# Kernel optimization log

Hardware: AMD Instinct MI355X
Metric: run time of the kernel (lower is better)

The kernel has to match this reference:

```python
import jax, jax.numpy as jnp
import numpy as np

N = 50000          # residues
E = 1000000        # edges
H = 128            # hidden_channels
CUT = 11.5         # cutoff
NR = 6             # num_radial
NS = 3             # num_spherical
NPE = 16           # num_pos_emb

def swish(x):
    return x * jax.nn.sigmoid(x)

def rbf(d):
    # Bessel-style radial basis with smooth cosine cutoff, [E, NR]
    u = jnp.clip(d / CUT, 0.0, 1.0)
    n = jnp.arange(1, NR + 1, dtype=jnp.float32)
    fc = 0.5 * (jnp.cos(jnp.pi * u) + 1.0)
    return jnp.sqrt(2.0 / CUT) * jnp.sin(n * jnp.pi * u[:, None]) / (d[:, None] + 1e-6) * fc[:, None]

def angle_emb(d, ang):
    # d_angle_emb: radial x cos(l*angle) -> [E, NR*NS]
    r = rbf(d)
    l = jnp.arange(NS, dtype=jnp.float32)
    a = jnp.cos(ang[:, None] * l)
    return (r[:, :, None] * a[:, None, :]).reshape(d.shape[0], NR * NS)

def theta_phi_emb(d, theta, phi):
    # d_theta_phi_emb: radial x angular(theta) x angular(phi) -> [E, NR*NS*NS]
    r = rbf(d)
    l = jnp.arange(NS, dtype=jnp.float32)
    ct = jnp.cos(theta[:, None] * l)
    cp = jnp.cos(phi[:, None] * l)
    return jnp.einsum('en,el,em->enlm', r, ct, cp).reshape(d.shape[0], NR * NS * NS)


def setup_inputs():
    key = jax.random.key(0)
    ks = jax.random.split(key, 20)
    f32 = jnp.float32
    pos = jax.random.normal(ks[0], (N, 3), f32) * 8.0
    pos_n = pos + jax.random.normal(ks[1], (N, 3), f32) * 0.8
    pos_c = pos + jax.random.normal(ks[2], (N, 3), f32) * 0.8
    z = jax.random.randint(ks[3], (N,), 0, 26)
    bb_embs = jax.random.normal(ks[4], (N, 6), f32)
    side_chain_embs = jax.random.normal(ks[5], (N, 8), f32)
    esm_embs = jax.random.normal(ks[6], (N, 1280), f32)
    batch = jnp.zeros((N,), jnp.int32)
    edge_index = jax.random.randint(ks[7], (2, E), 0, N)
    def w(k, shape):
        return jax.random.normal(k, shape, f32) * (1.0 / np.sqrt(shape[0]))
    edge_in = NR * NS * NS + 3 * NR * NS + NPE  # 54 + 54 + 16 = 124
    params = dict(
        W_emb=w(ks[8], (26 + 6 + 8, H // 2)), b_emb=jnp.zeros((H // 2,), f32),
        W_esm=w(ks[9], (1280, H // 2)), b_esm=jnp.zeros((H // 2,), f32),
        W_edge=w(ks[10], (edge_in, H)),
        W_msg=w(ks[11], (H, H)),
        W_upd=w(ks[12], (H, H)),
        W_o0=w(ks[13], (H, H)), b_o0=jnp.zeros((H,), f32),
        W_o1=w(ks[14], (H, 32)), b_o1=jnp.zeros((32,), f32),
        W_of=w(ks[15], (32, 1)), b_of=jnp.zeros((1,), f32),
        W_n0=w(ks[16], (H, 32)), b_n0=jnp.zeros((32,), f32),
        W_nf=w(ks[17], (32, 2)), b_nf=jnp.zeros((2,), f32),
    )
    return dict(z=z, pos=pos, pos_n=pos_n, pos_c=pos_c, bb_embs=bb_embs,
                side_chain_embs=side_chain_embs, esm_embs=esm_embs,
                batch=batch, edge_index=edge_index, **params)


def reference(z, pos, pos_n, pos_c, bb_embs, side_chain_embs, esm_embs, batch,
              edge_index, W_emb, b_emb, W_esm, b_esm, W_edge, W_msg, W_upd,
              W_o0, b_o0, W_o1, b_o1, W_of, b_of, W_n0, b_n0, W_nf, b_nf):
    # --- node embedding fusion (level='allatom+esm') ---
    oh = jax.nn.one_hot(z, 26, dtype=jnp.float32)
    x_a = jnp.concatenate([oh, bb_embs, side_chain_embs], axis=1) @ W_emb + b_emb
    x_s = esm_embs @ W_esm + b_esm
    x = jnp.concatenate([x_a, x_s], axis=-1)  # [N, H]

    j, i = edge_index[0], edge_index[1]

    # --- sinusoidal positional embedding of sequence offsets ---
    dpe = (j - i).astype(jnp.float32)
    freq = jnp.exp(jnp.arange(0, NPE, 2, dtype=jnp.float32) * (-np.log(10000.0) / NPE))
    ang = dpe[:, None] * freq
    pe = jnp.concatenate([jnp.cos(ang), jnp.sin(ang)], axis=-1)  # [E, NPE]

    # --- distance / theta / phi (triplet gathers via sequence neighbors) ---
    v_ji = pos[j] - pos[i]
    dist = jnp.linalg.norm(pos[i] - pos[j], axis=1)
    refi0 = (i - 1) % N
    refi1 = (i + 1) % N
    v_r0 = pos[refi0] - pos[i]
    v_r1 = pos[refi1] - pos[i]
    a = jnp.sum(v_ji * v_r0, axis=-1)
    b = jnp.linalg.norm(jnp.cross(v_ji, v_r0), axis=-1)
    theta = jnp.arctan2(b, a)
    p1 = jnp.cross(v_r0, v_r1)
    p2 = jnp.cross(v_r0, v_ji)
    a = jnp.sum(p1 * p2, axis=-1)
    b = jnp.sum(jnp.cross(p1, p2) * v_r0, axis=-1) / (jnp.linalg.norm(v_r0, axis=-1) + 1e-7)
    phi = jnp.arctan2(b, a)
    feature0 = theta_phi_emb(dist, theta, phi)  # [E, 54]

    # --- backbone-frame Euler angles (allatom branch) ---
    o1x = pos_n[i] - pos[i]
    o1z = jnp.cross(o1x, jnp.cross(o1x, pos_c[i] - pos[i]))
    o1zl = jnp.linalg.norm(o1z, axis=1) + 1e-7
    o2x = pos_n[j] - pos[j]
    o2z = jnp.cross(o2x, jnp.cross(o2x, pos_c[j] - pos[j]))
    o2zl = jnp.linalg.norm(o2z, axis=1) + 1e-7
    nvec = jnp.cross(o1z, o2z)
    angle1 = jnp.arctan2(jnp.sum(jnp.cross(o1x, nvec) * o1z, -1) / o1zl, jnp.sum(o1x * nvec, -1))
    angle2 = jnp.arctan2(jnp.linalg.norm(nvec, axis=-1), jnp.sum(o1z * o2z, -1))
    angle3 = jnp.arctan2(jnp.sum(jnp.cross(nvec, o2x) * o2z, -1) / o2zl, jnp.sum(nvec * o2x, -1))
    feature1 = jnp.concatenate([angle_emb(dist, angle1), angle_emb(dist, angle2),
                                angle_emb(dist, angle3)], axis=1)  # [E, 54]

    # --- message passing (gather-compute-scatter stand-in for model_E) ---
    ef = swish(jnp.concatenate([feature0, feature1, pe], axis=-1) @ W_edge)  # [E, H]
    m = swish(x[j] @ W_msg) * ef
    agg = jax.ops.segment_sum(m, i, num_segments=N)
    xe = x + swish(agg @ W_upd)

    # --- output heads (dropout inactive at inference) ---
    xn = jax.nn.relu(x @ W_n0 + b_n0)
    node_out = xn @ W_nf + b_nf                   # [N, 2]
    h = jax.nn.relu(xe @ W_o0 + b_o0)
    h = jax.nn.relu(h @ W_o1 + b_o1)
    out = jax.nn.sigmoid(h @ W_of + b_of)         # [N, 1]
    return out, node_out
```

## Files before the change

### kernel.cpp

```cpp
#include <hip/hip_runtime.h>
#include <math.h>
#include <stdint.h>

#define NRES 50000
#define NEDGE 1000000
#define PI_F 3.14159265358979323846f
#define NSEG 196

typedef __attribute__((ext_vector_type(8))) short short8;
typedef __attribute__((ext_vector_type(4))) float floatx4;
typedef __attribute__((ext_vector_type(2))) short bf16x2;
typedef __attribute__((address_space(1))) bf16x2* gbf16x2p;

struct f3 { float x, y, z; };
__device__ __forceinline__ f3 ld3(const float* __restrict__ p, int i) {
  return {p[3*i+0], p[3*i+1], p[3*i+2]};
}
__device__ __forceinline__ f3 f3sub(f3 a, f3 b){ return {a.x-b.x, a.y-b.y, a.z-b.z}; }
__device__ __forceinline__ f3 f3cross(f3 a, f3 b){
  return {a.y*b.z - a.z*b.y, a.z*b.x - a.x*b.z, a.x*b.y - a.y*b.x};
}
__device__ __forceinline__ float f3dot(f3 a, f3 b){ return a.x*b.x + a.y*b.y + a.z*b.z; }
__device__ __forceinline__ float swish_fast(float v){
  return v * __builtin_amdgcn_rcpf(1.0f + __expf(-v));
}
__device__ __forceinline__ short f2bf(float f){
  unsigned u = __float_as_uint(f);
  unsigned r = (u + 0x7fffu + ((u >> 16) & 1u)) >> 16;
  return (short)r;
}
__device__ __forceinline__ float bf2f(short s){
  return __uint_as_float(((unsigned)(unsigned short)s) << 16);
}
__device__ __forceinline__ float cos_atan2(float y, float x){
  return x * __builtin_amdgcn_rsqf(fmaxf(x*x + y*y, 1e-30f));
}
__device__ __forceinline__ void atom_pk_bf16(short* addr, bf16x2 v){
  __builtin_amdgcn_global_atomic_fadd_v2bf16((gbf16x2p)(uintptr_t)addr, v);
}
__device__ __forceinline__ unsigned pkbf(float lo, float hi){
  unsigned r;
  asm("v_cvt_pk_bf16_f32 %0, %1, %2" : "=v"(r) : "v"(lo), "v"(hi));
  return r;
}

__device__ __forceinline__ void edge_features(
    int e, int j, int i,
    const float* __restrict__ pos, const float* __restrict__ posn,
    const float* __restrict__ posc, short (*sF)[136])
{
  f3 pj = ld3(pos, j), pi = ld3(pos, i);
  f3 vji = f3sub(pj, pi);
  float nji2 = f3dot(vji, vji);
  float dist = sqrtf(nji2);
  int r0i = (i == 0) ? (NRES - 1) : (i - 1);
  int r1i = (i == NRES - 1) ? 0 : (i + 1);
  f3 vr0 = f3sub(ld3(pos, r0i), pi);
  f3 vr1 = f3sub(ld3(pos, r1i), pi);
  float nr02 = f3dot(vr0, vr0);

  float ct = f3dot(vji, vr0) * __builtin_amdgcn_rsqf(fmaxf(nji2 * nr02, 1e-30f));
  f3 p1 = f3cross(vr0, vr1);
  f3 p2 = f3cross(vr0, vji);
  float pa = f3dot(p1, p2);
  float pb = f3dot(f3cross(p1, p2), vr0) / (sqrtf(nr02) + 1e-7f);
  float cp = cos_atan2(pb, pa);

  f3 pni = ld3(posn, i), pci = ld3(posc, i);
  f3 o1x = f3sub(pni, pi);
  f3 o1z = f3cross(o1x, f3cross(o1x, f3sub(pci, pi)));
  float no1z2 = f3dot(o1z, o1z);
  float o1zl = sqrtf(no1z2) + 1e-7f;
  f3 pnj = ld3(posn, j), pcj = ld3(posc, j);
  f3 o2x = f3sub(pnj, pj);
  f3 o2z = f3cross(o2x, f3cross(o2x, f3sub(pcj, pj)));
  float no2z2 = f3dot(o2z, o2z);
  float o2zl = sqrtf(no2z2) + 1e-7f;
  f3 nv = f3cross(o1z, o2z);
  float y1 = f3dot(f3cross(o1x, nv), o1z) / o1zl;
  float ca1 = cos_atan2(y1, f3dot(o1x, nv));
  float ca2 = f3dot(o1z, o2z) * __builtin_amdgcn_rsqf(fmaxf(no1z2 * no2z2, 1e-30f));
  float y3 = f3dot(f3cross(nv, o2x), o2z) / o2zl;
  float ca3 = cos_atan2(y3, f3dot(nv, o2x));

  float u = fminf(dist * (1.0f/11.5f), 1.0f);
  float spu, cpu;
  __sincosf(PI_F * u, &spu, &cpu);
  float fc = 0.5f * (cpu + 1.0f);
  float pref = 0.41702882811414954f * __builtin_amdgcn_rcpf(dist + 1e-6f) * fc;
  float rb[6];
  {
    float twoc = 2.0f * cpu;
    float s_nm1 = 0.0f, s_n = spu;
    #pragma unroll
    for (int nn = 0; nn < 6; ++nn) {
      rb[nn] = pref * s_n;
      float s_np1 = twoc * s_n - s_nm1;
      s_nm1 = s_n; s_n = s_np1;
    }
  }

  float pend = 0.0f;
  float ctv[3] = {1.0f, ct, 2.0f*ct*ct - 1.0f};
  float cpv[3] = {1.0f, cp, 2.0f*cp*cp - 1.0f};
  #pragma unroll
  for (int nn = 0; nn < 6; ++nn)
    #pragma unroll
    for (int l = 0; l < 3; ++l)
      #pragma unroll
      for (int m = 0; m < 3; ++m) {
        const int f = nn*9 + l*3 + m;
        float v = rb[nn] * ctv[l] * cpv[m];
        if (f & 1) *(unsigned*)&sF[e][f-1] = pkbf(pend, v);
        else       pend = v;
      }

  float cas[3] = {ca1, ca2, ca3};
  #pragma unroll
  for (int t = 0; t < 3; ++t) {
    float c = cas[t];
    float cav[3] = {1.0f, c, 2.0f*c*c - 1.0f};
    #pragma unroll
    for (int nn = 0; nn < 6; ++nn)
      #pragma unroll
      for (int l = 0; l < 3; ++l) {
        const int f = 54 + t*18 + nn*3 + l;
        float v = rb[nn] * cav[l];
        if (f & 1) *(unsigned*)&sF[e][f-1] = pkbf(pend, v);
        else       pend = v;
      }
  }

  const float FRQ[8] = {1.0f, 0.31622776601683794f, 0.1f, 0.03162277660168379f,
                        0.01f, 0.003162277660168379f, 0.001f, 0.0003162277660168379f};
  float dpe = (float)(j - i);
  float cb[8], sb[8];
  #pragma unroll
  for (int q = 0; q < 8; ++q) __sincosf(dpe * FRQ[q], &sb[q], &cb[q]);
  #pragma unroll
  for (int q = 0; q < 8; q += 2) {
    *(unsigned*)&sF[e][108 + q] = pkbf(cb[q], cb[q+1]);
    *(unsigned*)&sF[e][116 + q] = pkbf(sb[q], sb[q+1]);
  }
  *(unsigned*)&sF[e][124] = 0u;
  *(unsigned*)&sF[e][126] = 0u;
}

__global__ __launch_bounds__(256) void k_wprep(
    const float* __restrict__ We, const float* __restrict__ Wm,
    const float* __restrict__ Ws, const float* __restrict__ Wu,
    const float* __restrict__ Wo0, const float* __restrict__ Wn0,
    const float* __restrict__ Wo1,
    short* __restrict__ Wef, short* __restrict__ Wmf, short* __restrict__ Wsf,
    short* __restrict__ Wuf, short* __restrict__ Wo0f,
    short* __restrict__ Wn0f, short* __restrict__ Wo1f)
{
  int gid = blockIdx.x * 256 + threadIdx.x;
  const float* src; short* dst; int NT, K, N, t;
  if      (gid < 16384)  { t = gid;          src = We;  dst = Wef;  NT = 8; K = 124;  N = 128; }
  else if (gid < 32768)  { t = gid - 16384;  src = Wm;  dst = Wmf;  NT = 8; K = 128;  N = 128; }
  else if (gid < 114688) { t = gid - 32768;  src = Ws;  dst = Wsf;  NT = 4; K = 1280; N = 64;  }
  else if (gid < 131072) { t = gid - 114688; src = Wu;  dst = Wuf;  NT = 8; K = 128;  N = 128; }
  else if (gid < 147456) { t = gid - 131072; src = Wo0; dst = Wo0f; NT = 8; K = 128;  N = 128; }
  else if (gid < 151552) { t = gid - 147456; src = Wn0; dst = Wn0f; NT = 2; K = 128;  N = 32;  }
  else if (gid < 155648) { t = gid - 151552; src = Wo1; dst = Wo1f; NT = 2; K = 128;  N = 32;  }
  else return;
  int j = t & 7, lane = (t >> 3) & 63;
  int rest = t >> 9;
  int nt = rest % NT, kt = rest / NT;
  int k = kt*32 + (lane >> 4)*8 + j, n = nt*16 + (lane & 15);
  dst[t] = f2bf((k < K) ? src[k*N + n] : 0.0f);
}

__global__ __launch_bounds__(256) void k_hist(
    const int* __restrict__ ei, int* __restrict__ bins)
{
  int e = blockIdx.x * 256 + threadIdx.x;
  if (e < NEDGE) atomicAdd(&bins[ei[NEDGE + e]], 1);
}

__global__ __launch_bounds__(256) void k_scan1(
    int* __restrict__ bins, int* __restrict__ bsum)
{
  __shared__ int s[256];
  const int t = threadIdx.x, b = blockIdx.x;
  const int idx = b * 256 + t;
  int v = (idx < NRES) ? bins[idx] : 0;
  s[t] = v;
  __syncthreads();
  #pragma unroll
  for (int d = 1; d < 256; d <<= 1) {
    int add = (t >= d) ? s[t - d] : 0;
    __syncthreads();
    if (t >= d) s[t] += add;
    __syncthreads();
  }
  if (idx < NRES) bins[idx] = s[t] - v;
  if (t == 255) bsum[b] = s[255];
}

__global__ __launch_bounds__(256) void k_scan2(int* __restrict__ bsum)
{
  __shared__ int s[256];
  const int t = threadIdx.x;
  int v = (t < NSEG) ? bsum[t] : 0;
  s[t] = v;
  __syncthreads();
  #pragma unroll
  for (int d = 1; d < 256; d <<= 1) {
    int add = (t >= d) ? s[t - d] : 0;
    __syncthreads();
    if (t >= d) s[t] += add;
    __syncthreads();
  }
  if (t < NSEG) bsum[t] = s[t] - v;
}

__global__ __launch_bounds__(256) void k_scan3(
    int* __restrict__ bins, const int* __restrict__ bsum)
{
  int idx = blockIdx.x * 256 + threadIdx.x;
  if (idx < NRES) bins[idx] += bsum[blockIdx.x];
}

__global__ __launch_bounds__(256) void k_scatter(
    const int* __restrict__ ei, int* __restrict__ bins, int2* __restrict__ sij)
{
  int e = blockIdx.x * 256 + threadIdx.x;
  if (e < NEDGE) {
    int j = ei[e], i = ei[NEDGE + e];
    int slot = atomicAdd(&bins[i], 1);
    if (slot >= 0 && slot < NEDGE) sij[slot] = make_int2(j, i);
  }
}

__global__ __launch_bounds__(256) void k_xa(
    const int* __restrict__ z, const float* __restrict__ bb,
    const float* __restrict__ side, const float* __restrict__ W_emb,
    const float* __restrict__ b_emb, short* __restrict__ xb)
{
  int tid = threadIdx.x;
  int h = tid & 63;
  int n = blockIdx.x * 4 + (tid >> 6);
  if (n >= NRES) return;
  int zz = z[n];
  float acc = W_emb[zz * 64 + h] + b_emb[h];
  #pragma unroll
  for (int k = 0; k < 6; ++k) acc += bb[n*6 + k] * W_emb[(26 + k)*64 + h];
  #pragma unroll
  for (int k = 0; k < 8; ++k) acc += side[n*8 + k] * W_emb[(32 + k)*64 + h];
  xb[(size_t)n * 128 + h] = f2bf(acc);
}

__global__ __launch_bounds__(256) void k_esm(
    const float* __restrict__ esm, const short* __restrict__ Wsf,
    const float* __restrict__ b, short* __restrict__ xb)
{
  const int tid = threadIdx.x;
  const int lane = tid & 63, w = tid >> 6;
  const int quad = lane >> 4, colb = lane & 15;
  const int tile0 = blockIdx.x * 64 + w * 16;

  int arow = tile0 + colb;
  if (arow >= NRES) arow = NRES - 1;
  const float* ap = esm + (size_t)arow * 1280 + quad * 8;

  floatx4 acc[4];
  #pragma unroll
  for (int nt = 0; nt < 4; ++nt) acc[nt] = (floatx4){0.f, 0.f, 0.f, 0.f};

  for (int kt = 0; kt < 40; ++kt) {
    float4 v0 = *(const float4*)(ap + kt*32);
    float4 v1 = *(const float4*)(ap + kt*32 + 4);
    short8 a;
    a[0] = f2bf(v0.x); a[1] = f2bf(v0.y); a[2] = f2bf(v0.z); a[3] = f2bf(v0.w);
    a[4] = f2bf(v1.x); a[5] = f2bf(v1.y); a[6] = f2bf(v1.z); a[7] = f2bf(v1.w);
    #pragma unroll
    for (int nt = 0; nt < 4; ++nt) {
      short8 bf = *(const short8*)&Wsf[(size_t)((kt*4 + nt)*64 + lane)*8];
      acc[nt] = __builtin_amdgcn_mfma_f32_16x16x32_bf16(a, bf, acc[nt], 0, 0, 0);
    }
  }
  #pragma unroll
  for (int nt = 0; nt < 4; ++nt) {
    int ch = nt*16 + colb;
    float bias = b[ch];
    #pragma unroll
    for (int r = 0; r < 4; ++r) {
      int n = tile0 + quad*4 + r;
      if (n < NRES) xb[(size_t)n * 128 + 64 + ch] = f2bf(acc[nt][r] + bias);
    }
  }
}

__global__ __launch_bounds__(512) void k_node(
    const float* __restrict__ esm, const short* __restrict__ Wsf,
    const float* __restrict__ b_esm,
    const int* __restrict__ z, const float* __restrict__ bb,
    const float* __restrict__ side, const float* __restrict__ W_emb,
    const float* __restrict__ b_emb,
    const short* __restrict__ Wmf,
    short* __restrict__ xb, short* __restrict__ xmb)
{
  __shared__ __align__(16) short sX[64][136];
  __shared__ float sP[4][16][68];

  const int tid = threadIdx.x;
  const int lane = tid & 63, w = tid >> 6;
  const int quad = lane >> 4, colb = lane & 15;
  const int t = w & 3, kh = w >> 2;
  const int n0 = blockIdx.x * 64;
  const int tile0 = n0 + t * 16;

  int arow = tile0 + colb;
  if (arow >= NRES) arow = NRES - 1;
  const float* ap = esm + (size_t)arow * 1280 + kh * 640 + quad * 8;

  floatx4 acc[4];
  #pragma unroll
  for (int nt = 0; nt < 4; ++nt) acc[nt] = (floatx4){0.f, 0.f, 0.f, 0.f};

  float4 v0 = *(const float4*)(ap);
  float4 v1 = *(const float4*)(ap + 4);
  for (int kt = 0; kt < 20; ++kt) {
    float4 nv0 = v0, nv1 = v1;
    if (kt < 19) {
      nv0 = *(const float4*)(ap + (kt+1)*32);
      nv1 = *(const float4*)(ap + (kt+1)*32 + 4);
    }
    short8 a;
    a[0] = f2bf(v0.x); a[1] = f2bf(v0.y); a[2] = f2bf(v0.z); a[3] = f2bf(v0.w);
    a[4] = f2bf(v1.x); a[5] = f2bf(v1.y); a[6] = f2bf(v1.z); a[7] = f2bf(v1.w);
    const int kc = kh*20 + kt;
    #pragma unroll
    for (int nt = 0; nt < 4; ++nt) {
      short8 bf = *(const short8*)&Wsf[(size_t)((kc*4 + nt)*64 + lane)*8];
      acc[nt] = __builtin_amdgcn_mfma_f32_16x16x32_bf16(a, bf, acc[nt], 0, 0, 0);
    }
    v0 = nv0; v1 = nv1;
  }

  if (kh == 1) {
    #pragma unroll
    for (int nt = 0; nt < 4; ++nt)
      #pragma unroll
      for (int r = 0; r < 4; ++r)
        sP[t][quad*4 + r][nt*16 + colb] = acc[nt][r];
  }
  __syncthreads();

  if (kh == 0) {
    #pragma unroll
    for (int nt = 0; nt < 4; ++nt) {
      int ch = nt*16 + colb;
      float bias = b_esm[ch];
      #pragma unroll
      for (int r = 0; r < 4; ++r)
        sX[t*16 + quad*4 + r][64 + ch] =
            f2bf(acc[nt][r] + sP[t][quad*4 + r][ch] + bias);
    }
  }
  {
    int r2 = tid >> 3;
    int n2 = n0 + r2; if (n2 >= NRES) n2 = NRES - 1;
    int c0 = (tid & 7) * 8;
    int zz = z[n2];
    float bbv[6], sdv[8];
    #pragma unroll
    for (int k = 0; k < 6; ++k) bbv[k] = bb[n2*6 + k];
    #pragma unroll
    for (int k = 0; k < 8; ++k) sdv[k] = side[n2*8 + k];
    #pragma unroll
    for (int c = 0; c < 8; c += 2) {
      float u0, u1;
      #pragma unroll
      for (int h = 0; h < 2; ++h) {
        int col = c0 + c + h;
        float a2 = W_emb[zz*64 + col] + b_emb[col];
        #pragma unroll
        for (int k = 0; k < 6; ++k) a2 += bbv[k] * W_emb[(26 + k)*64 + col];
        #pragma unroll
        for (int k = 0; k < 8; ++k) a2 += sdv[k] * W_emb[(32 + k)*64 + col];
        if (h) u1 = a2; else u0 = a2;
      }
      *(unsigned*)&sX[r2][c0 + c] = pkbf(u0, u1);
    }
  }
  __syncthreads();

  #pragma unroll
  for (int it = 0; it < 2; ++it) {
    int idx = it * 512 + tid;
    int row = idx >> 4, c8 = idx & 15;
    int n = n0 + row;
    if (n < NRES) *(short8*)&xb[(size_t)n * 128 + c8*8] = *(const short8*)&sX[row][c8*8];
  }

  floatx4 accM[4];
  #pragma unroll
  for (int mt = 0; mt < 4; ++mt) accM[mt] = (floatx4){0.f,0.f,0.f,0.f};
  #pragma unroll
  for (int kt = 0; kt < 4; ++kt) {
    short8 b0 = *(const short8*)&Wmf[(size_t)((kt*8 + w)*64 + lane)*8];
    #pragma unroll
    for (int mt = 0; mt < 4; ++mt) {
      short8 a = *(const short8*)&sX[mt*16 + colb][kt*32 + quad*8];
      accM[mt] = __builtin_amdgcn_mfma_f32_16x16x32_bf16(a, b0, accM[mt], 0, 0, 0);
    }
  }
  __syncthreads();

  #pragma unroll
  for (int mt = 0; mt < 4; ++mt)
    #pragma unroll
    for (int r = 0; r < 4; ++r)
      sX[mt*16 + quad*4 + r][w*16 + colb] = f2bf(swish_fast(accM[mt][r]));
  __syncthreads();
  #pragma unroll
  for (int it = 0; it < 2; ++it) {
    int idx = it * 512 + tid;
    int row = idx >> 4, c8 = idx & 15;
    int n = n0 + row;
    if (n < NRES) *(short8*)&xmb[(size_t)n * 128 + c8*8] = *(const short8*)&sX[row][c8*8];
  }
}

__global__ __launch_bounds__(256, 4) void k_edge_s(
    const int2* __restrict__ sij,
    const float* __restrict__ pos,
    const float* __restrict__ posn, const float* __restrict__ posc,
    const short* __restrict__ xmb, const short* __restrict__ Wef,
    short* __restrict__ aggb)
{
  __shared__ int sJ[64];
  __shared__ int sI[64];
  __shared__ __align__(16) short sF[64][136];
  __shared__ __align__(16) short sXJ[64][136];

  const int tid = threadIdx.x;
  const int orig = blockIdx.x;
  const int xcd = orig & 7, sub = orig >> 3;
  const int wg = (xcd == 0 ? 0 : 1954 + (xcd - 1) * 1953) + sub;
  const int e0 = wg * 64;

  if (tid < 64) {
    int2 ji = sij[e0 + tid];
    int jj = ji.x, ii = ji.y;
    sJ[tid] = (jj < 0) ? 0 : ((jj >= NRES) ? NRES - 1 : jj);
    sI[tid] = (ii < 0) ? 0 : ((ii >= NRES) ? NRES - 1 : ii);
  }
  __syncthreads();

  if (tid < 64) {
    edge_features(tid, sJ[tid], sI[tid], pos, posn, posc, sF);
  } else {
    const int t2 = tid - 64;
    for (int it = 0; it < 6; ++it) {
      int idx = it * 192 + t2;
      if (idx < 1024) {
        int row = idx >> 4;
        int c8 = idx & 15;
        *(short8*)&sXJ[row][c8*8] = *(const short8*)&xmb[(size_t)sJ[row] * 128 + c8*8];
      }
    }
  }
  __syncthreads();

  const int lane = tid & 63, w = tid >> 6;
  const int quad = lane >> 4, colb = lane & 15;
  const int nb = w * 2;

  short8 bE[4][2];
  #pragma unroll
  for (int kt = 0; kt < 4; ++kt)
    #pragma unroll
    for (int nt = 0; nt < 2; ++nt)
      bE[kt][nt] = *(const short8*)&Wef[(size_t)((kt*8 + nb + nt)*64 + lane)*8];

  floatx4 accE[4][2];
  #pragma unroll
  for (int mt = 0; mt < 4; ++mt) {
    accE[mt][0] = (floatx4){0.f, 0.f, 0.f, 0.f};
    accE[mt][1] = (floatx4){0.f, 0.f, 0.f, 0.f};
  }

  #pragma unroll
  for (int kt = 0; kt < 4; ++kt) {
    #pragma unroll
    for (int mt = 0; mt < 4; ++mt) {
      short8 af = *(const short8*)&sF[mt*16 + colb][kt*32 + quad*8];
      #pragma unroll
      for (int nt = 0; nt < 2; ++nt)
        accE[mt][nt] = __builtin_amdgcn_mfma_f32_16x16x32_bf16(af, bE[kt][nt], accE[mt][nt], 0, 0, 0);
    }
  }
  __syncthreads();

  short (*sM)[136] = sF;
  #pragma unroll
  for (int mt = 0; mt < 4; ++mt)
    #pragma unroll
    for (int nt = 0; nt < 2; ++nt) {
      int ch = w*32 + nt*16 + colb;
      #pragma unroll
      for (int r = 0; r < 4; ++r) {
        int e = mt*16 + quad*4 + r;
        float mv = bf2f(sXJ[e][ch]) * swish_fast(accE[mt][nt][r]);
        sM[e][ch] = f2bf(mv);
      }
    }
  __syncthreads();

  {
    const int p = tid & 63;
    const int g = tid >> 6;
    float ax = 0.f, ay = 0.f;
    int cur = sI[g * 16];
    #pragma unroll
    for (int rr = 0; rr < 16; ++rr) {
      int row = g * 16 + rr;
      int ii = sI[row];
      if (ii != cur) {
        bf16x2 v; v[0] = f2bf(ax); v[1] = f2bf(ay);
        atom_pk_bf16(&aggb[(size_t)cur * 128 + p*2], v);
        ax = 0.f; ay = 0.f; cur = ii;
      }
      bf16x2 mv = *(const bf16x2*)&sM[row][p*2];
      ax += bf2f(mv[0]); ay += bf2f(mv[1]);
    }
    bf16x2 v; v[0] = f2bf(ax); v[1] = f2bf(ay);
    atom_pk_bf16(&aggb[(size_t)cur * 128 + p*2], v);
  }
}

__global__ __launch_bounds__(256, 4) void k_edge_b(
    const int* __restrict__ ei, const float* __restrict__ pos,
    const float* __restrict__ posn, const float* __restrict__ posc,
    const short* __restrict__ xb, const short* __restrict__ Wef,
    const short* __restrict__ Wmf, short* __restrict__ aggb)
{
  __shared__ int sJ[64];
  __shared__ int sI[64];
  __shared__ __align__(16) short sF[64][136];
  __shared__ __align__(16) short sXJ[64][136];

  const int tid = threadIdx.x;
  const int e0 = blockIdx.x * 64;

  if (tid < 64) { sJ[tid] = ei[e0 + tid]; sI[tid] = ei[NEDGE + e0 + tid]; }
  __syncthreads();

  if (tid < 64) {
    edge_features(tid, sJ[tid], sI[tid], pos, posn, posc, sF);
  } else {
    const int t2 = tid - 64;
    for (int it = 0; it < 6; ++it) {
      int idx = it * 192 + t2;
      if (idx < 1024) {
        int row = idx >> 4;
        int c8 = idx & 15;
        *(short8*)&sXJ[row][c8*8] = *(const short8*)&xb[(size_t)sJ[row] * 128 + c8*8];
      }
    }
  }
  __syncthreads();

  const int lane = tid & 63, w = tid >> 6;
  const int quad = lane >> 4, colb = lane & 15;
  const int nb = w * 2;

  short8 bE[4][2], bM[4][2];
  #pragma unroll
  for (int kt = 0; kt < 4; ++kt)
    #pragma unroll
    for (int nt = 0; nt < 2; ++nt) {
      bE[kt][nt] = *(const short8*)&Wef[(size_t)((kt*8 + nb + nt)*64 + lane)*8];
      bM[kt][nt] = *(const short8*)&Wmf[(size_t)((kt*8 + nb + nt)*64 + lane)*8];
    }

  floatx4 accE[4][2], accM[4][2];
  #pragma unroll
  for (int mt = 0; mt < 4; ++mt)
    #pragma unroll
    for (int nt = 0; nt < 2; ++nt) {
      accE[mt][nt] = (floatx4){0.f, 0.f, 0.f, 0.f};
      accM[mt][nt] = (floatx4){0.f, 0.f, 0.f, 0.f};
    }

  #pragma unroll
  for (int kt = 0; kt < 4; ++kt) {
    #pragma unroll
    for (int mt = 0; mt < 4; ++mt) {
      short8 af = *(const short8*)&sF [mt*16 + colb][kt*32 + quad*8];
      short8 ax = *(const short8*)&sXJ[mt*16 + colb][kt*32 + quad*8];
      #pragma unroll
      for (int nt = 0; nt < 2; ++nt) {
        accE[mt][nt] = __builtin_amdgcn_mfma_f32_16x16x32_bf16(af, bE[kt][nt], accE[mt][nt], 0, 0, 0);
        accM[mt][nt] = __builtin_amdgcn_mfma_f32_16x16x32_bf16(ax, bM[kt][nt], accM[mt][nt], 0, 0, 0);
      }
    }
  }
  __syncthreads();

  short (*sM)[136] = sXJ;
  #pragma unroll
  for (int mt = 0; mt < 4; ++mt)
    #pragma unroll
    for (int nt = 0; nt < 2; ++nt) {
      int ch = w*32 + nt*16 + colb;
      #pragma unroll
      for (int r = 0; r < 4; ++r) {
        int e = mt*16 + quad*4 + r;
        sM[e][ch] = f2bf(swish_fast(accM[mt][nt][r]) * swish_fast(accE[mt][nt][r]));
      }
    }
  __syncthreads();

  #pragma unroll
  for (int it = 0; it < 16; ++it) {
    int flat = it * 256 + tid;
    int row = flat >> 6, p = flat & 63;
    bf16x2 v = *(const bf16x2*)&sM[row][p*2];
    atom_pk_bf16(&aggb[(size_t)sI[row] * 128 + p*2], v);
  }
}

__global__ __launch_bounds__(256) void k_upd(
    const short* __restrict__ xb, const short* __restrict__ aggb,
    const short* __restrict__ Wuf, const short* __restrict__ Wo0f,
    const short* __restrict__ Wn0f, const short* __restrict__ Wo1f,
    const float* __restrict__ bn0, const float* __restrict__ Wnf,
    const float* __restrict__ bnf, const float* __restrict__ bo0,
    const float* __restrict__ bo1, const float* __restrict__ Wof,
    const float* __restrict__ bof, float* __restrict__ out0,
    float* __restrict__ out1)
{
  __shared__ __align__(16) short sA[64][136];
  __shared__ __align__(16) short sX[64][136];
  __shared__ float sS[64][33];

  const int tid = threadIdx.x;
  const int lane = tid & 63, w = tid >> 6;
  const int quad = lane >> 4, colb = lane & 15;
  const int n0 = blockIdx.x * 64;

  #pragma unroll
  for (int it = 0; it < 4; ++it) {
    int idx = it * 256 + tid;
    int row = idx >> 4, c8 = idx & 15;
    int n = n0 + row;
    short8 va = (short8)(short)0, vx = (short8)(short)0;
    if (n < NRES) {
      va = *(const short8*)&aggb[(size_t)n * 128 + c8*8];
      vx = *(const short8*)&xb  [(size_t)n * 128 + c8*8];
    }
    *(short8*)&sA[row][c8*8] = va;
    *(short8*)&sX[row][c8*8] = vx;
  }
  __syncthreads();

  {
    floatx4 accN[2];
    accN[0] = (floatx4){0.f,0.f,0.f,0.f}; accN[1] = (floatx4){0.f,0.f,0.f,0.f};
    #pragma unroll
    for (int kt = 0; kt < 4; ++kt) {
      short8 a = *(const short8*)&sX[w*16 + colb][kt*32 + quad*8];
      #pragma unroll
      for (int nt = 0; nt < 2; ++nt) {
        short8 bf = *(const short8*)&Wn0f[(size_t)((kt*2 + nt)*64 + lane)*8];
        accN[nt] = __builtin_amdgcn_mfma_f32_16x16x32_bf16(a, bf, accN[nt], 0, 0, 0);
      }
    }
    #pragma unroll
    for (int nt = 0; nt < 2; ++nt) {
      int col = nt*16 + colb;
      float bias = bn0[col];
      #pragma unroll
      for (int r = 0; r < 4; ++r)
        sS[w*16 + quad*4 + r][col] = fmaxf(accN[nt][r] + bias, 0.0f);
    }
  }
  __syncthreads();
  if (tid < 128) {
    int row = tid >> 1, oc = tid & 1;
    int n = n0 + row;
    if (n < NRES) {
      float a2 = bnf[oc];
      #pragma unroll
      for (int k = 0; k < 32; ++k) a2 += sS[row][k] * Wnf[k*2 + oc];
      out1[(size_t)n * 2 + oc] = a2;
    }
  }

  floatx4 acc1[4][2];
  #pragma unroll
  for (int mt = 0; mt < 4; ++mt) {
    acc1[mt][0] = (floatx4){0.f,0.f,0.f,0.f};
    acc1[mt][1] = (floatx4){0.f,0.f,0.f,0.f};
  }
  #pragma unroll
  for (int kt = 0; kt < 4; ++kt) {
    short8 b0 = *(const short8*)&Wuf[(size_t)((kt*8 + w*2 + 0)*64 + lane)*8];
    short8 b1 = *(const short8*)&Wuf[(size_t)((kt*8 + w*2 + 1)*64 + lane)*8];
    #pragma unroll
    for (int mt = 0; mt < 4; ++mt) {
      short8 a = *(const short8*)&sA[mt*16 + colb][kt*32 + quad*8];
      acc1[mt][0] = __builtin_amdgcn_mfma_f32_16x16x32_bf16(a, b0, acc1[mt][0], 0, 0, 0);
      acc1[mt][1] = __builtin_amdgcn_mfma_f32_16x16x32_bf16(a, b1, acc1[mt][1], 0, 0, 0);
    }
  }
  __syncthreads();
  #pragma unroll
  for (int mt = 0; mt < 4; ++mt)
    #pragma unroll
    for (int nt = 0; nt < 2; ++nt)
      #pragma unroll
      for (int r = 0; r < 4; ++r) {
        int row = mt*16 + quad*4 + r, col = w*32 + nt*16 + colb;
        float xv = bf2f(sX[row][col]);
        sA[row][col] = f2bf(xv + swish_fast(acc1[mt][nt][r]));
      }
  __syncthreads();

  floatx4 acc2[4][2];
  #pragma unroll
  for (int mt = 0; mt < 4; ++mt) {
    acc2[mt][0] = (floatx4){0.f,0.f,0.f,0.f};
    acc2[mt][1] = (floatx4){0.f,0.f,0.f,0.f};
  }
  #pragma unroll
  for (int kt = 0; kt < 4; ++kt) {
    short8 b0 = *(const short8*)&Wo0f[(size_t)((kt*8 + w*2 + 0)*64 + lane)*8];
    short8 b1 = *(const short8*)&Wo0f[(size_t)((kt*8 + w*2 + 1)*64 + lane)*8];
    #pragma unroll
    for (int mt = 0; mt < 4; ++mt) {
      short8 a = *(const short8*)&sA[mt*16 + colb][kt*32 + quad*8];
      acc2[mt][0] = __builtin_amdgcn_mfma_f32_16x16x32_bf16(a, b0, acc2[mt][0], 0, 0, 0);
      acc2[mt][1] = __builtin_amdgcn_mfma_f32_16x16x32_bf16(a, b1, acc2[mt][1], 0, 0, 0);
    }
  }
  __syncthreads();
  #pragma unroll
  for (int mt = 0; mt < 4; ++mt)
    #pragma unroll
    for (int nt = 0; nt < 2; ++nt) {
      int col = w*32 + nt*16 + colb;
      float bias = bo0[col];
      #pragma unroll
      for (int r = 0; r < 4; ++r) {
        int row = mt*16 + quad*4 + r;
        sX[row][col] = f2bf(fmaxf(acc2[mt][nt][r] + bias, 0.0f));
      }
    }
  __syncthreads();

  {
    floatx4 accH[2];
    accH[0] = (floatx4){0.f,0.f,0.f,0.f}; accH[1] = (floatx4){0.f,0.f,0.f,0.f};
    #pragma unroll
    for (int kt = 0; kt < 4; ++kt) {
      short8 a = *(const short8*)&sX[w*16 + colb][kt*32 + quad*8];
      #pragma unroll
      for (int nt = 0; nt < 2; ++nt) {
        short8 bf = *(const short8*)&Wo1f[(size_t)((kt*2 + nt)*64 + lane)*8];
        accH[nt] = __builtin_amdgcn_mfma_f32_16x16x32_bf16(a, bf, accH[nt], 0, 0, 0);
      }
    }
    __syncthreads();
    #pragma unroll
    for (int nt = 0; nt < 2; ++nt) {
      int col = nt*16 + colb;
      float bias = bo1[col];
      #pragma unroll
      for (int r = 0; r < 4; ++r)
        sS[w*16 + quad*4 + r][col] = fmaxf(accH[nt][r] + bias, 0.0f);
    }
  }
  __syncthreads();

  if (tid < 64) {
    int n = n0 + tid;
    if (n < NRES) {
      float a2 = bof[0];
      #pragma unroll
      for (int k = 0; k < 32; ++k) a2 += sS[tid][k] * Wof[k];
      out0[n] = 1.0f / (1.0f + expf(-a2));
    }
  }
}

extern "C" void kernel_launch(void* const* d_in, const int* in_sizes, int n_in,
                              void* d_out, int out_size, void* d_ws, size_t ws_size,
                              hipStream_t stream) {
  (void)in_sizes; (void)n_in; (void)out_size;
  const int*   z     = (const int*)  d_in[0];
  const float* pos   = (const float*)d_in[1];
  const float* posn  = (const float*)d_in[2];
  const float* posc  = (const float*)d_in[3];
  const float* bb    = (const float*)d_in[4];
  const float* side  = (const float*)d_in[5];
  const float* esm   = (const float*)d_in[6];
  const int*   ei    = (const int*)  d_in[8];
  const float* W_emb = (const float*)d_in[9];
  const float* b_emb = (const float*)d_in[10];
  const float* W_esm = (const float*)d_in[11];
  const float* b_esm = (const float*)d_in[12];
  const float* W_edge= (const float*)d_in[13];
  const float* W_msg = (const float*)d_in[14];
  const float* W_upd = (const float*)d_in[15];
  const float* W_o0  = (const float*)d_in[16];
  const float* b_o0  = (const float*)d_in[17];
  const float* W_o1  = (const float*)d_in[18];
  const float* b_o1  = (const float*)d_in[19];
  const float* W_of  = (const float*)d_in[20];
  const float* b_of  = (const float*)d_in[21];
  const float* W_n0  = (const float*)d_in[22];
  const float* b_n0  = (const float*)d_in[23];
  const float* W_nf  = (const float*)d_in[24];
  const float* b_nf  = (const float*)d_in[25];

  float* out0 = (float*)d_out;
  float* out1 = out0 + NRES;
  char* ws = (char*)d_ws;

  const bool full = (ws_size >= (size_t)46912096);

  if (full) {
    short* xb   = (short*)ws;
    short* aggb = (short*)(ws + 12800000);
    short* xmb  = (short*)(ws + 25600000);
    short* Wef  = (short*)(ws + 38400000);
    short* Wmf  = (short*)(ws + 38432768);
    short* Wsf  = (short*)(ws + 38465536);
    short* Wuf  = (short*)(ws + 38629376);
    short* Wo0f = (short*)(ws + 38662144);
    short* Wn0f = (short*)(ws + 38694912);
    short* Wo1f = (short*)(ws + 38703104);
    int*   bins = (int*)  (ws + 38711296);
    int*   bsum = (int*)  (ws + 38911296);
    int2*  sij  = (int2*) (ws + 38912096);

    hipMemsetAsync(aggb, 0, (size_t)NRES * 128 * sizeof(short), stream);
    hipMemsetAsync(bins, 0, (size_t)NRES * sizeof(int), stream);

    k_wprep  <<<608, 256, 0, stream>>>(W_edge, W_msg, W_esm, W_upd, W_o0, W_n0, W_o1,
                                       Wef, Wmf, Wsf, Wuf, Wo0f, Wn0f, Wo1f);
    k_hist   <<<3907, 256, 0, stream>>>(ei, bins);
    k_scan1  <<<NSEG, 256, 0, stream>>>(bins, bsum);
    k_scan2  <<<1,    256, 0, stream>>>(bsum);
    k_scan3  <<<NSEG, 256, 0, stream>>>(bins, bsum);
    k_scatter<<<3907, 256, 0, stream>>>(ei, bins, sij);
    k_node   <<<782,  512, 0, stream>>>(esm, Wsf, b_esm, z, bb, side, W_emb, b_emb,
                                        Wmf, xb, xmb);
    k_edge_s <<<15625, 256, 0, stream>>>(sij, pos, posn, posc, xmb, Wef, aggb);
    k_upd    <<<782,   256, 0, stream>>>(xb, aggb, Wuf, Wo0f, Wn0f, Wo1f,
                                         b_n0, W_nf, b_nf, b_o0, b_o1, W_of, b_of,
                                         out0, out1);
  } else {
    short* xb   = (short*)ws;
    short* aggb = (short*)(ws + 12800000);
    short* Wef  = (short*)(ws + 25600000);
    short* Wmf  = (short*)(ws + 25632768);
    short* Wsf  = (short*)(ws + 25665536);
    short* Wuf  = (short*)(ws + 25829376);
    short* Wo0f = (short*)(ws + 25862144);
    short* Wn0f = (short*)(ws + 25894912);
    short* Wo1f = (short*)(ws + 25903104);

    hipMemsetAsync(aggb, 0, (size_t)NRES * 128 * sizeof(short), stream);

    k_wprep <<<608, 256, 0, stream>>>(W_edge, W_msg, W_esm, W_upd, W_o0, W_n0, W_o1,
                                      Wef, Wmf, Wsf, Wuf, Wo0f, Wn0f, Wo1f);
    k_xa    <<<12500, 256, 0, stream>>>(z, bb, side, W_emb, b_emb, xb);
    k_esm   <<<782,   256, 0, stream>>>(esm, Wsf, b_esm, xb);
    k_edge_b<<<15625, 256, 0, stream>>>(ei, pos, posn, posc, xb, Wef, Wmf, aggb);
    k_upd   <<<782,   256, 0, stream>>>(xb, aggb, Wuf, Wo0f, Wn0f, Wo1f,
                                        b_n0, W_nf, b_nf, b_o0, b_o1, W_of, b_of,
                                        out0, out1);
  }
}
```

Before: 706.7 us.

## Split edge feature work across all warps, restage ESM GEMM, fold scan3 into scatter

In the sorted-edge kernel, each edge's features are now computed by four threads. Every thread recomputes the geometry and then writes one quarter of the feature row, replacing the old scheme where a single warp did all the feature math while the others gathered xmb. The node kernel's ESM projection now stages bf16-converted ESM rows in double-buffered shared memory with a 4x2 warp tiling over rows and columns, replacing the split-K approach and its partial-sum reduction. The k_scan3 launch is removed by adding the block offset during the scatter atomic. The cost is that the geometry is recomputed four times per edge, and the node kernel gains extra barriers.

```diff
diff --git a/kernel.cpp b/kernel.cpp
--- a/kernel.cpp
+++ b/kernel.cpp
@@ -44,11 +44,17 @@
   return r;
 }
 
-__device__ __forceinline__ void edge_features(
-    int e, int j, int i,
+struct EdgeGeo {
+  float rb[6];
+  float ct, cp, ca1, ca2, ca3;
+  float dpe;
+};
+__device__ __forceinline__ EdgeGeo edge_geo(
+    int j, int i,
     const float* __restrict__ pos, const float* __restrict__ posn,
-    const float* __restrict__ posc, short (*sF)[136])
-{
+    const float* __restrict__ posc)
+{
+  EdgeGeo g;
   f3 pj = ld3(pos, j), pi = ld3(pos, i);
   f3 vji = f3sub(pj, pi);
   float nji2 = f3dot(vji, vji);
@@ -59,12 +65,12 @@
   f3 vr1 = f3sub(ld3(pos, r1i), pi);
   float nr02 = f3dot(vr0, vr0);
 
-  float ct = f3dot(vji, vr0) * __builtin_amdgcn_rsqf(fmaxf(nji2 * nr02, 1e-30f));
+  g.ct = f3dot(vji, vr0) * __builtin_amdgcn_rsqf(fmaxf(nji2 * nr02, 1e-30f));
   f3 p1 = f3cross(vr0, vr1);
   f3 p2 = f3cross(vr0, vji);
   float pa = f3dot(p1, p2);
   float pb = f3dot(f3cross(p1, p2), vr0) / (sqrtf(nr02) + 1e-7f);
-  float cp = cos_atan2(pb, pa);
+  g.cp = cos_atan2(pb, pa);
 
   f3 pni = ld3(posn, i), pci = ld3(posc, i);
   f3 o1x = f3sub(pni, pi);
@@ -78,65 +84,68 @@
   float o2zl = sqrtf(no2z2) + 1e-7f;
   f3 nv = f3cross(o1z, o2z);
   float y1 = f3dot(f3cross(o1x, nv), o1z) / o1zl;
-  float ca1 = cos_atan2(y1, f3dot(o1x, nv));
-  float ca2 = f3dot(o1z, o2z) * __builtin_amdgcn_rsqf(fmaxf(no1z2 * no2z2, 1e-30f));
+  g.ca1 = cos_atan2(y1, f3dot(o1x, nv));
+  g.ca2 = f3dot(o1z, o2z) * __builtin_amdgcn_rsqf(fmaxf(no1z2 * no2z2, 1e-30f));
   float y3 = f3dot(f3cross(nv, o2x), o2z) / o2zl;
-  float ca3 = cos_atan2(y3, f3dot(nv, o2x));
+  g.ca3 = cos_atan2(y3, f3dot(nv, o2x));
 
   float u = fminf(dist * (1.0f/11.5f), 1.0f);
   float spu, cpu;
   __sincosf(PI_F * u, &spu, &cpu);
   float fc = 0.5f * (cpu + 1.0f);
   float pref = 0.41702882811414954f * __builtin_amdgcn_rcpf(dist + 1e-6f) * fc;
-  float rb[6];
   {
     float twoc = 2.0f * cpu;
     float s_nm1 = 0.0f, s_n = spu;
     #pragma unroll
     for (int nn = 0; nn < 6; ++nn) {
-      rb[nn] = pref * s_n;
+      g.rb[nn] = pref * s_n;
       float s_np1 = twoc * s_n - s_nm1;
       s_nm1 = s_n; s_n = s_np1;
     }
   }
-
-  float pend = 0.0f;
-  float ctv[3] = {1.0f, ct, 2.0f*ct*ct - 1.0f};
-  float cpv[3] = {1.0f, cp, 2.0f*cp*cp - 1.0f};
-  #pragma unroll
-  for (int nn = 0; nn < 6; ++nn)
-    #pragma unroll
-    for (int l = 0; l < 3; ++l)
-      #pragma unroll
-      for (int m = 0; m < 3; ++m) {
-        const int f = nn*9 + l*3 + m;
-        float v = rb[nn] * ctv[l] * cpv[m];
-        if (f & 1) *(unsigned*)&sF[e][f-1] = pkbf(pend, v);
-        else       pend = v;
-      }
-
-  float cas[3] = {ca1, ca2, ca3};
-  #pragma unroll
-  for (int t = 0; t < 3; ++t) {
-    float c = cas[t];
-    float cav[3] = {1.0f, c, 2.0f*c*c - 1.0f};
-    #pragma unroll
-    for (int nn = 0; nn < 6; ++nn)
-      #pragma unroll
-      for (int l = 0; l < 3; ++l) {
-        const int f = 54 + t*18 + nn*3 + l;
-        float v = rb[nn] * cav[l];
-        if (f & 1) *(unsigned*)&sF[e][f-1] = pkbf(pend, v);
-        else       pend = v;
-      }
-  }
-
+  g.dpe = (float)(j - i);
+  return g;
+}
+
+__device__ __forceinline__ float feat_val(const EdgeGeo& g, int f,
+                                          const float* ctv, const float* cpv,
+                                          const float* cav1, const float* cav2,
+                                          const float* cav3)
+{
+  if (f < 54) {
+    int nn = f / 9, l = (f % 9) / 3, m = f % 3;
+    return g.rb[nn] * ctv[l] * cpv[m];
+  } else {
+    int ff = f - 54;
+    int t = ff / 18, nn = (ff % 18) / 3, l = ff % 3;
+    const float* cav = (t == 0) ? cav1 : (t == 1) ? cav2 : cav3;
+    return g.rb[nn] * cav[l];
+  }
+}
+
+__device__ __forceinline__ void edge_features_full(
+    int e, int j, int i,
+    const float* __restrict__ pos, const float* __restrict__ posn,
+    const float* __restrict__ posc, short (*sF)[136])
+{
+  EdgeGeo g = edge_geo(j, i, pos, posn, posc);
+  float ctv[3]  = {1.0f, g.ct,  2.0f*g.ct*g.ct  - 1.0f};
+  float cpv[3]  = {1.0f, g.cp,  2.0f*g.cp*g.cp  - 1.0f};
+  float cav1[3] = {1.0f, g.ca1, 2.0f*g.ca1*g.ca1 - 1.0f};
+  float cav2[3] = {1.0f, g.ca2, 2.0f*g.ca2*g.ca2 - 1.0f};
+  float cav3[3] = {1.0f, g.ca3, 2.0f*g.ca3*g.ca3 - 1.0f};
+  #pragma unroll
+  for (int f = 0; f < 108; f += 2) {
+    float v0 = feat_val(g, f,     ctv, cpv, cav1, cav2, cav3);
+    float v1 = feat_val(g, f + 1, ctv, cpv, cav1, cav2, cav3);
+    *(unsigned*)&sF[e][f] = pkbf(v0, v1);
+  }
   const float FRQ[8] = {1.0f, 0.31622776601683794f, 0.1f, 0.03162277660168379f,
                         0.01f, 0.003162277660168379f, 0.001f, 0.0003162277660168379f};
-  float dpe = (float)(j - i);
   float cb[8], sb[8];
   #pragma unroll
-  for (int q = 0; q < 8; ++q) __sincosf(dpe * FRQ[q], &sb[q], &cb[q]);
+  for (int q = 0; q < 8; ++q) __sincosf(g.dpe * FRQ[q], &sb[q], &cb[q]);
   #pragma unroll
   for (int q = 0; q < 8; q += 2) {
     *(unsigned*)&sF[e][108 + q] = pkbf(cb[q], cb[q+1]);
@@ -144,6 +153,53 @@
   }
   *(unsigned*)&sF[e][124] = 0u;
   *(unsigned*)&sF[e][126] = 0u;
+}
+
+__device__ __forceinline__ void edge_features_q(
+    int e, int j, int i, int q,
+    const float* __restrict__ pos, const float* __restrict__ posn,
+    const float* __restrict__ posc, short (*sF)[136])
+{
+  EdgeGeo g = edge_geo(j, i, pos, posn, posc);
+  float ctv[3]  = {1.0f, g.ct,  2.0f*g.ct*g.ct  - 1.0f};
+  float cpv[3]  = {1.0f, g.cp,  2.0f*g.cp*g.cp  - 1.0f};
+  float cav1[3] = {1.0f, g.ca1, 2.0f*g.ca1*g.ca1 - 1.0f};
+  float cav2[3] = {1.0f, g.ca2, 2.0f*g.ca2*g.ca2 - 1.0f};
+  float cav3[3] = {1.0f, g.ca3, 2.0f*g.ca3*g.ca3 - 1.0f};
+
+  if (q == 0) {
+    #pragma unroll
+    for (int f = 0; f < 28; f += 2)
+      *(unsigned*)&sF[e][f] = pkbf(feat_val(g, f, ctv, cpv, cav1, cav2, cav3),
+                                   feat_val(g, f+1, ctv, cpv, cav1, cav2, cav3));
+  } else if (q == 1) {
+    #pragma unroll
+    for (int f = 28; f < 54; f += 2)
+      *(unsigned*)&sF[e][f] = pkbf(feat_val(g, f, ctv, cpv, cav1, cav2, cav3),
+                                   feat_val(g, f+1, ctv, cpv, cav1, cav2, cav3));
+    const float FRQ[8] = {1.0f, 0.31622776601683794f, 0.1f, 0.03162277660168379f,
+                          0.01f, 0.003162277660168379f, 0.001f, 0.0003162277660168379f};
+    float cb[8], sb[8];
+    #pragma unroll
+    for (int p = 0; p < 8; ++p) __sincosf(g.dpe * FRQ[p], &sb[p], &cb[p]);
+    #pragma unroll
+    for (int p = 0; p < 8; p += 2) {
+      *(unsigned*)&sF[e][108 + p] = pkbf(cb[p], cb[p+1]);
+      *(unsigned*)&sF[e][116 + p] = pkbf(sb[p], sb[p+1]);
+    }
+    *(unsigned*)&sF[e][124] = 0u;
+    *(unsigned*)&sF[e][126] = 0u;
+  } else if (q == 2) {
+    #pragma unroll
+    for (int f = 54; f < 80; f += 2)
+      *(unsigned*)&sF[e][f] = pkbf(feat_val(g, f, ctv, cpv, cav1, cav2, cav3),
+                                   feat_val(g, f+1, ctv, cpv, cav1, cav2, cav3));
+  } else {
+    #pragma unroll
+    for (int f = 80; f < 108; f += 2)
+      *(unsigned*)&sF[e][f] = pkbf(feat_val(g, f, ctv, cpv, cav1, cav2, cav3),
+                                   feat_val(g, f+1, ctv, cpv, cav1, cav2, cav3));
+  }
 }
 
 __global__ __launch_bounds__(256) void k_wprep(
@@ -216,20 +272,14 @@
   if (t < NSEG) bsum[t] = s[t] - v;
 }
 
-__global__ __launch_bounds__(256) void k_scan3(
-    int* __restrict__ bins, const int* __restrict__ bsum)
-{
-  int idx = blockIdx.x * 256 + threadIdx.x;
-  if (idx < NRES) bins[idx] += bsum[blockIdx.x];
-}
-
 __global__ __launch_bounds__(256) void k_scatter(
-    const int* __restrict__ ei, int* __restrict__ bins, int2* __restrict__ sij)
+    const int* __restrict__ ei, int* __restrict__ bins,
+    const int* __restrict__ bsum, int2* __restrict__ sij)
 {
   int e = blockIdx.x * 256 + threadIdx.x;
   if (e < NEDGE) {
     int j = ei[e], i = ei[NEDGE + e];
-    int slot = atomicAdd(&bins[i], 1);
+    int slot = atomicAdd(&bins[i], 1) + bsum[i >> 8];
     if (slot >= 0 && slot < NEDGE) sij[slot] = make_int2(j, i);
   }
 }
@@ -302,62 +352,70 @@
     const short* __restrict__ Wmf,
     short* __restrict__ xb, short* __restrict__ xmb)
 {
+  __shared__ __align__(16) short sE[2][64][72];
   __shared__ __align__(16) short sX[64][136];
-  __shared__ float sP[4][16][68];
 
   const int tid = threadIdx.x;
   const int lane = tid & 63, w = tid >> 6;
   const int quad = lane >> 4, colb = lane & 15;
-  const int t = w & 3, kh = w >> 2;
   const int n0 = blockIdx.x * 64;
-  const int tile0 = n0 + t * 16;
-
-  int arow = tile0 + colb;
-  if (arow >= NRES) arow = NRES - 1;
-  const float* ap = esm + (size_t)arow * 1280 + kh * 640 + quad * 8;
-
-  floatx4 acc[4];
-  #pragma unroll
-  for (int nt = 0; nt < 4; ++nt) acc[nt] = (floatx4){0.f, 0.f, 0.f, 0.f};
-
-  float4 v0 = *(const float4*)(ap);
-  float4 v1 = *(const float4*)(ap + 4);
-  for (int kt = 0; kt < 20; ++kt) {
-    float4 nv0 = v0, nv1 = v1;
-    if (kt < 19) {
-      nv0 = *(const float4*)(ap + (kt+1)*32);
-      nv1 = *(const float4*)(ap + (kt+1)*32 + 4);
-    }
-    short8 a;
-    a[0] = f2bf(v0.x); a[1] = f2bf(v0.y); a[2] = f2bf(v0.z); a[3] = f2bf(v0.w);
-    a[4] = f2bf(v1.x); a[5] = f2bf(v1.y); a[6] = f2bf(v1.z); a[7] = f2bf(v1.w);
-    const int kc = kh*20 + kt;
-    #pragma unroll
-    for (int nt = 0; nt < 4; ++nt) {
-      short8 bf = *(const short8*)&Wsf[(size_t)((kc*4 + nt)*64 + lane)*8];
-      acc[nt] = __builtin_amdgcn_mfma_f32_16x16x32_bf16(a, bf, acc[nt], 0, 0, 0);
-    }
-    v0 = nv0; v1 = nv1;
-  }
-
-  if (kh == 1) {
-    #pragma unroll
-    for (int nt = 0; nt < 4; ++nt)
-      #pragma unroll
-      for (int r = 0; r < 4; ++r)
-        sP[t][quad*4 + r][nt*16 + colb] = acc[nt][r];
-  }
-  __syncthreads();
-
-  if (kh == 0) {
-    #pragma unroll
-    for (int nt = 0; nt < 4; ++nt) {
-      int ch = nt*16 + colb;
-      float bias = b_esm[ch];
-      #pragma unroll
-      for (int r = 0; r < 4; ++r)
-        sX[t*16 + quad*4 + r][64 + ch] =
-            f2bf(acc[nt][r] + sP[t][quad*4 + r][ch] + bias);
+
+  const int lrow = tid >> 3;
+  const int p0 = tid & 7, p1 = p0 + 8;
+  int grow = n0 + lrow; if (grow >= NRES) grow = NRES - 1;
+  const float* rbase = esm + (size_t)grow * 1280;
+
+  const int rt = w & 3;
+  const int ct0 = (w >> 2) * 2, ct1 = ct0 + 1;
+
+  floatx4 acc0 = (floatx4){0.f,0.f,0.f,0.f};
+  floatx4 acc1 = (floatx4){0.f,0.f,0.f,0.f};
+
+  {
+    float4 va = *(const float4*)(rbase + p0*4);
+    float4 vb = *(const float4*)(rbase + p1*4);
+    *(unsigned*)&sE[0][lrow][p0*4]     = pkbf(va.x, va.y);
+    *(unsigned*)&sE[0][lrow][p0*4 + 2] = pkbf(va.z, va.w);
+    *(unsigned*)&sE[0][lrow][p1*4]     = pkbf(vb.x, vb.y);
+    *(unsigned*)&sE[0][lrow][p1*4 + 2] = pkbf(vb.z, vb.w);
+  }
+  __syncthreads();
+
+  for (int s = 0; s < 20; ++s) {
+    float4 va = {0.f,0.f,0.f,0.f}, vb = {0.f,0.f,0.f,0.f};
+    if (s < 19) {
+      va = *(const float4*)(rbase + (s+1)*64 + p0*4);
+      vb = *(const float4*)(rbase + (s+1)*64 + p1*4);
+    }
+    const int buf = s & 1;
+    #pragma unroll
+    for (int kk = 0; kk < 2; ++kk) {
+      short8 af = *(const short8*)&sE[buf][rt*16 + colb][kk*32 + quad*8];
+      const int kc = s*2 + kk;
+      short8 bf0 = *(const short8*)&Wsf[(size_t)((kc*4 + ct0)*64 + lane)*8];
+      short8 bf1 = *(const short8*)&Wsf[(size_t)((kc*4 + ct1)*64 + lane)*8];
+      acc0 = __builtin_amdgcn_mfma_f32_16x16x32_bf16(af, bf0, acc0, 0, 0, 0);
+      acc1 = __builtin_amdgcn_mfma_f32_16x16x32_bf16(af, bf1, acc1, 0, 0, 0);
+    }
+    __syncthreads();
+    if (s < 19) {
+      const int nb = (s + 1) & 1;
+      *(unsigned*)&sE[nb][lrow][p0*4]     = pkbf(va.x, va.y);
+      *(unsigned*)&sE[nb][lrow][p0*4 + 2] = pkbf(va.z, va.w);
+      *(unsigned*)&sE[nb][lrow][p1*4]     = pkbf(vb.x, vb.y);
+      *(unsigned*)&sE[nb][lrow][p1*4 + 2] = pkbf(vb.z, vb.w);
+      __syncthreads();
+    }
+  }
+
+  {
+    float bias0 = b_esm[ct0*16 + colb];
+    float bias1 = b_esm[ct1*16 + colb];
+    #pragma unroll
+    for (int r = 0; r < 4; ++r) {
+      int row = rt*16 + quad*4 + r;
+      sX[row][64 + ct0*16 + colb] = f2bf(acc0[r] + bias0);
+      sX[row][64 + ct1*16 + colb] = f2bf(acc1[r] + bias1);
     }
   }
   {
@@ -451,18 +509,16 @@
   }
   __syncthreads();
 
-  if (tid < 64) {
-    edge_features(tid, sJ[tid], sI[tid], pos, posn, posc, sF);
-  } else {
-    const int t2 = tid - 64;
-    for (int it = 0; it < 6; ++it) {
-      int idx = it * 192 + t2;
-      if (idx < 1024) {
-        int row = idx >> 4;
-        int c8 = idx & 15;
-        *(short8*)&sXJ[row][c8*8] = *(const short8*)&xmb[(size_t)sJ[row] * 128 + c8*8];
-      }
-    }
+  {
+    const int e = tid & 63, q = tid >> 6;
+    edge_features_q(e, sJ[e], sI[e], q, pos, posn, posc, sF);
+  }
+  #pragma unroll
+  for (int it = 0; it < 4; ++it) {
+    int idx = it * 256 + tid;
+    int row = idx >> 4;
+    int c8 = idx & 15;
+    *(short8*)&sXJ[row][c8*8] = *(const short8*)&xmb[(size_t)sJ[row] * 128 + c8*8];
   }
   __syncthreads();
 
@@ -551,7 +607,7 @@
   __syncthreads();
 
   if (tid < 64) {
-    edge_features(tid, sJ[tid], sI[tid], pos, posn, posc, sF);
+    edge_features_full(tid, sJ[tid], sI[tid], pos, posn, posc, sF);
   } else {
     const int t2 = tid - 64;
     for (int it = 0; it < 6; ++it) {
@@ -848,8 +904,7 @@
     k_hist   <<<3907, 256, 0, stream>>>(ei, bins);
     k_scan1  <<<NSEG, 256, 0, stream>>>(bins, bsum);
     k_scan2  <<<1,    256, 0, stream>>>(bsum);
-    k_scan3  <<<NSEG, 256, 0, stream>>>(bins, bsum);
-    k_scatter<<<3907, 256, 0, stream>>>(ei, bins, sij);
+    k_scatter<<<3907, 256, 0, stream>>>(ei, bins, bsum, sij);
     k_node   <<<782,  512, 0, stream>>>(esm, Wsf, b_esm, z, bb, side, W_emb, b_emb,
                                         Wmf, xb, xmb);
     k_edge_s <<<15625, 256, 0, stream>>>(sij, pos, posn, posc, xmb, Wef, aggb);
```

Result: faster. 675.5 us (-4.4%).
